# Optimization experiments

Hardware: AMD Instinct MI355X
Metric: run time of the kernel (lower is better)

The kernel has to match this reference:

```python
import jax, jax.numpy as jnp
import numpy as np

D = 128
N0, N1, N2 = 1048576, 131072, 8192   # node counts per sampled layer (src->tgt)
E0, E1 = 1048576, 131072             # edges per layer


def setup_inputs() -> dict:
    key = jax.random.key(0)
    ks = jax.random.split(key, 11)
    s = 1.0 / np.sqrt(D)  # torch Linear init scale
    u = lambda k: jax.random.uniform(k, (D, D), jnp.float32, -s, s)
    return {
        "x": jax.random.normal(ks[0], (N0, D), jnp.float32),
        "Wl0": u(ks[1]), "bl0": jnp.zeros((D,), jnp.float32), "Wr0": u(ks[2]),
        "Wl1": u(ks[3]), "bl1": jnp.zeros((D,), jnp.float32), "Wr1": u(ks[4]),
        "src0": jax.random.randint(ks[5], (E0,), 0, N0, jnp.int32),
        "dst0": jax.random.randint(ks[6], (E0,), 0, N1, jnp.int32),
        "src1": jax.random.randint(ks[7], (E1,), 0, N1, jnp.int32),
        "dst1": jax.random.randint(ks[8], (E1,), 0, N2, jnp.int32),
    }


def _sage_conv(x_src, x_tgt, src, dst, Wl, bl, Wr, n_tgt):
    # message: gather source features along edges; aggregate: mean per target
    msg = x_src[src]                                        # [E, D]
    agg = jax.ops.segment_sum(msg, dst, num_segments=n_tgt)  # [n_tgt, D]
    cnt = jax.ops.segment_sum(jnp.ones((src.shape[0], 1), x_src.dtype),
                              dst, num_segments=n_tgt)       # [n_tgt, 1]
    mean = agg / jnp.maximum(cnt, 1.0)                      # zero-degree -> 0
    return mean @ Wl + bl + x_tgt @ Wr


def reference(x, Wl0, bl0, Wr0, Wl1, bl1, Wr1, src0, dst0, src1, dst1):
    # layer 0: N0 sources -> N1 targets
    h = _sage_conv(x, x[:N1], src0, dst0, Wl0, bl0, Wr0, N1)
    h = jax.nn.relu(h)  # dropout p=0.0 is identity
    # layer 1: N1 sources -> N2 targets
    h = _sage_conv(h, h[:N2], src1, dst1, Wl1, bl1, Wr1, N2)
    return jax.nn.relu(h)
```

## Files before the change

kernel.cpp:

```cpp
#include <hip/hip_runtime.h>
#include <hip/hip_bf16.h>

#define D 128
#define N0_ 1048576
#define N1_ 131072
#define N2_ 8192
#define E0_ 1048576
#define E1_ 131072

typedef float f32x4 __attribute__((ext_vector_type(4)));
typedef short bf16x8 __attribute__((ext_vector_type(8)));
typedef unsigned short u16x4 __attribute__((ext_vector_type(4)));

__device__ __forceinline__ short f2bf(float f) {
    __hip_bfloat16 h = __float2bfloat16(f);
    return __builtin_bit_cast(short, h);
}
__device__ __forceinline__ float bf2f(short s) {
    return __bfloat162float(__builtin_bit_cast(__hip_bfloat16, s));
}

__global__ __launch_bounds__(256) void zero_kernel(int4* __restrict__ p, int n4) {
    int i = blockIdx.x * 256 + threadIdx.x;
    if (i < n4) p[i] = int4{0, 0, 0, 0};
}

__global__ __launch_bounds__(256) void hist_both(const int* __restrict__ dst0,
                                                 const int* __restrict__ dst1,
                                                 int* __restrict__ deg) {
    int g = blockIdx.x * 256 + threadIdx.x;
    if (g < E0_ / 4) {
        int4 d4 = ((const int4*)dst0)[g];
        atomicAdd(&deg[d4.x], 1);
        atomicAdd(&deg[d4.y], 1);
        atomicAdd(&deg[d4.z], 1);
        atomicAdd(&deg[d4.w], 1);
    } else {
        int4 d4 = ((const int4*)dst1)[g - E0_ / 4];
        atomicAdd(&deg[N1_ + d4.x], 1);
        atomicAdd(&deg[N1_ + d4.y], 1);
        atomicAdd(&deg[N1_ + d4.z], 1);
        atomicAdd(&deg[N1_ + d4.w], 1);
    }
}

__global__ __launch_bounds__(256) void scan1(const int* __restrict__ deg,
                                             int* __restrict__ offs,
                                             int* __restrict__ bsum, int n) {
    __shared__ int ws[4];
    int i = blockIdx.x * 256 + threadIdx.x;
    int lane = threadIdx.x & 63, wid = threadIdx.x >> 6;
    int v = (i < n) ? deg[i] : 0;
    int incl = v;
#pragma unroll
    for (int d = 1; d < 64; d <<= 1) {
        int u = __shfl_up(incl, d);
        if (lane >= d) incl += u;
    }
    if (lane == 63) ws[wid] = incl;
    __syncthreads();
    if (threadIdx.x == 0) {
        int a = 0;
        for (int w = 0; w < 4; ++w) { int t = ws[w]; ws[w] = a; a += t; }
        bsum[blockIdx.x] = a;
    }
    __syncthreads();
    if (i < n) offs[i] = incl - v + ws[wid];
}

__global__ __launch_bounds__(1024) void scan2(int* __restrict__ bsum, int nb) {
    __shared__ int ws[16];
    int i = threadIdx.x, lane = i & 63, wid = i >> 6;
    int v = (i < nb) ? bsum[i] : 0;
    int incl = v;
#pragma unroll
    for (int d = 1; d < 64; d <<= 1) {
        int u = __shfl_up(incl, d);
        if (lane >= d) incl += u;
    }
    if (lane == 63) ws[wid] = incl;
    __syncthreads();
    if (i == 0) {
        int a = 0;
        for (int w = 0; w < 16; ++w) { int t = ws[w]; ws[w] = a; a += t; }
    }
    __syncthreads();
    if (i < nb) bsum[i] = incl - v + ws[wid];
}

__global__ __launch_bounds__(256) void scan3(int* __restrict__ offs,
                                             const int* __restrict__ bsum, int n) {
    int i = blockIdx.x * 256 + threadIdx.x;
    if (i < n) offs[i] += bsum[blockIdx.x];
}

__global__ __launch_bounds__(256) void scatter_both(const int* __restrict__ src0,
                                                    const int* __restrict__ dst0,
                                                    const int* __restrict__ src1,
                                                    const int* __restrict__ dst1,
                                                    int* __restrict__ offs,
                                                    int* __restrict__ eidx0,
                                                    int* __restrict__ eidx1) {
    int g = blockIdx.x * 256 + threadIdx.x;
    if (g < E0_ / 4) {
        int4 s4 = ((const int4*)src0)[g];
        int4 d4 = ((const int4*)dst0)[g];
        int p;
        p = atomicAdd(&offs[d4.x], 1); eidx0[p] = s4.x;
        p = atomicAdd(&offs[d4.y], 1); eidx0[p] = s4.y;
        p = atomicAdd(&offs[d4.z], 1); eidx0[p] = s4.z;
        p = atomicAdd(&offs[d4.w], 1); eidx0[p] = s4.w;
    } else {
        int gq = g - E0_ / 4;
        int4 s4 = ((const int4*)src1)[gq];
        int4 d4 = ((const int4*)dst1)[gq];
        int p;
        p = atomicAdd(&offs[N1_ + d4.x], 1); eidx1[p - E0_] = s4.x;
        p = atomicAdd(&offs[N1_ + d4.y], 1); eidx1[p - E0_] = s4.y;
        p = atomicAdd(&offs[N1_ + d4.z], 1); eidx1[p - E0_] = s4.z;
        p = atomicAdd(&offs[N1_ + d4.w], 1); eidx1[p - E0_] = s4.w;
    }
}

template <bool SRCBF16>
__device__ __forceinline__ f32x4 row_load4(const void* xsrc_v, int s, int hl) {
    if (SRCBF16) {
        const short* xs = (const short*)xsrc_v;
        u16x4 v = ((const u16x4*)(xs + (size_t)s * D))[hl];
        f32x4 r;
        r[0] = bf2f((short)v[0]); r[1] = bf2f((short)v[1]);
        r[2] = bf2f((short)v[2]); r[3] = bf2f((short)v[3]);
        return r;
    } else {
        const float* xs = (const float*)xsrc_v;
        return ((const f32x4*)(xs + (size_t)s * D))[hl];
    }
}

template <bool SRCBF16>
__global__ __launch_bounds__(256) void aggregate(const void* __restrict__ xsrc_v,
                                                 const int* __restrict__ eidx,
                                                 const int* __restrict__ offs_end,
                                                 const int* __restrict__ deg,
                                                 int joint_base, int eidx_sub,
                                                 short* __restrict__ mean, int ntgt) {
    const int lane = threadIdx.x & 63;
    const int half = lane >> 5, hl = lane & 31;
    const int gw = (blockIdx.x * 256 + threadIdx.x) >> 6;
    const int nw = (gridDim.x * 256) >> 6;
    for (int t = gw; t < ntgt; t += nw) {
        const int tj = joint_base + t;
        const int dgr = deg[tj];
        const int start = offs_end[tj] - dgr - eidx_sub;
        f32x4 acc = {0.0f, 0.0f, 0.0f, 0.0f};
        for (int base = 0; base < dgr; base += 64) {
            const int nc = min(64, dgr - base);
            int sidx = (lane < nc) ? eidx[start + base + lane] : 0;
            int i = 0;
            for (; i + 8 <= nc; i += 8) {
                f32x4 v[4];
#pragma unroll
                for (int u = 0; u < 4; ++u) {
                    int s0 = __shfl(sidx, i + 2 * u);
                    int s1 = __shfl(sidx, i + 2 * u + 1);
                    v[u] = row_load4<SRCBF16>(xsrc_v, half ? s1 : s0, hl);
                }
#pragma unroll
                for (int u = 0; u < 4; ++u) acc += v[u];
            }
            for (; i + 2 <= nc; i += 2) {
                int s0 = __shfl(sidx, i);
                int s1 = __shfl(sidx, i + 1);
                acc += row_load4<SRCBF16>(xsrc_v, half ? s1 : s0, hl);
            }
            if (i < nc) {
                int s0 = __shfl(sidx, i);
                if (half == 0) acc += row_load4<SRCBF16>(xsrc_v, s0, hl);
            }
        }
#pragma unroll
        for (int c = 0; c < 4; ++c) acc[c] += __shfl_xor(acc[c], 32);
        const float r = (dgr > 0) ? 1.0f / (float)dgr : 0.0f;
        if (half == 0) {
            u16x4 o;
#pragma unroll
            for (int c = 0; c < 4; ++c) o[c] = (unsigned short)f2bf(acc[c] * r);
            ((u16x4*)(mean + (size_t)t * D))[hl] = o;
        }
    }
}

template <bool XBF16, bool OUTBF16>
__global__ __launch_bounds__(256) void sage_update(
    const short* __restrict__ mean, const void* __restrict__ xtgt_v,
    const float* __restrict__ Wl, const float* __restrict__ Wr,
    const float* __restrict__ bl, void* __restrict__ out_v, int ntiles) {
    __shared__ __align__(16) char wt[128 * 256 * 2];

    {
        int t = threadIdx.x;
        int j = t & 127;
        int half = t >> 7;
        const float* W = half ? Wr : Wl;
        for (int k = 0; k < 128; ++k) {
            float v = W[k * 128 + j];
            int kk = half * 128 + k;
            int byte = (j * 512 + kk * 2) ^ ((j & 7) << 4);
            *reinterpret_cast<short*>(wt + byte) = f2bf(v);
        }
    }
    __syncthreads();

    const int wave = threadIdx.x >> 6, lane = threadIdx.x & 63;
    const int rl = lane & 15;
    const int kq = lane >> 4;

    float blv[8];
#pragma unroll
    for (int nt = 0; nt < 8; ++nt) blv[nt] = bl[nt * 16 + rl];

    for (int tile = blockIdx.x; tile < ntiles; tile += gridDim.x) {
        const int grow = tile * 64 + wave * 16 + rl;
        f32x4 acc[8] = {};

#pragma unroll
        for (int ks = 0; ks < 8; ++ks) {
            const int k0 = ks * 32 + kq * 8;
            bf16x8 af;
            if (ks < 4) {
                af = *reinterpret_cast<const bf16x8*>(mean + (size_t)grow * D + k0);
            } else {
                const int kx = k0 - 128;
                if (XBF16) {
                    af = *reinterpret_cast<const bf16x8*>(
                        (const short*)xtgt_v + (size_t)grow * D + kx);
                } else {
                    const float4* p = reinterpret_cast<const float4*>(
                        (const float*)xtgt_v + (size_t)grow * D + kx);
                    float4 a = p[0], b = p[1];
                    af[0] = f2bf(a.x); af[1] = f2bf(a.y);
                    af[2] = f2bf(a.z); af[3] = f2bf(a.w);
                    af[4] = f2bf(b.x); af[5] = f2bf(b.y);
                    af[6] = f2bf(b.z); af[7] = f2bf(b.w);
                }
            }
#pragma unroll
            for (int nt = 0; nt < 8; ++nt) {
                const int j = nt * 16 + rl;
                const int byte = (j * 512 + k0 * 2) ^ ((j & 7) << 4);
                bf16x8 bfr = *reinterpret_cast<const bf16x8*>(wt + byte);
                acc[nt] =
                    __builtin_amdgcn_mfma_f32_16x16x32_bf16(af, bfr, acc[nt], 0, 0, 0);
            }
        }

        const int orow_base = tile * 64 + wave * 16 + kq * 4;
#pragma unroll
        for (int nt = 0; nt < 8; ++nt) {
            const int col = nt * 16 + rl;
#pragma unroll
            for (int r = 0; r < 4; ++r) {
                float v = acc[nt][r] + blv[nt];
                v = fmaxf(v, 0.0f);
                const size_t idx = (size_t)(orow_base + r) * D + col;
                if (OUTBF16)
                    ((short*)out_v)[idx] = f2bf(v);
                else
                    ((float*)out_v)[idx] = v;
            }
        }
    }
}

extern "C" void kernel_launch(void* const* d_in, const int* in_sizes, int n_in,
                              void* d_out, int out_size, void* d_ws, size_t ws_size,
                              hipStream_t stream) {
    const float* x   = (const float*)d_in[0];
    const float* Wl0 = (const float*)d_in[1];
    const float* bl0 = (const float*)d_in[2];
    const float* Wr0 = (const float*)d_in[3];
    const float* Wl1 = (const float*)d_in[4];
    const float* bl1 = (const float*)d_in[5];
    const float* Wr1 = (const float*)d_in[6];
    const int* src0  = (const int*)d_in[7];
    const int* dst0  = (const int*)d_in[8];
    const int* src1  = (const int*)d_in[9];
    const int* dst1  = (const int*)d_in[10];

    char* ws = (char*)d_ws;
    int*   deg   = (int*)(ws);
    int*   offs  = (int*)(ws + 557056);
    int*   bsum  = (int*)(ws + 1114112);
    int*   eidx0 = (int*)(ws + 1118208);
    int*   eidx1 = (int*)(ws + 5312512);
    short* mean0 = (short*)(ws + 5836800);
    short* mean1 = (short*)(ws + 39391232);
    short* h     = (short*)(ws + 41488384);

    const int NJ = N1_ + N2_;

    zero_kernel<<<136, 256, 0, stream>>>((int4*)deg, NJ / 4);
    hist_both<<<(E0_ + E1_) / 1024, 256, 0, stream>>>(dst0, dst1, deg);
    scan1<<<NJ / 256, 256, 0, stream>>>(deg, offs, bsum, NJ);
    scan2<<<1, 1024, 0, stream>>>(bsum, NJ / 256);
    scan3<<<NJ / 256, 256, 0, stream>>>(offs, bsum, NJ);
    scatter_both<<<(E0_ + E1_) / 1024, 256, 0, stream>>>(src0, dst0, src1, dst1,
                                                         offs, eidx0, eidx1);

    aggregate<false><<<4096, 256, 0, stream>>>(x, eidx0, offs, deg, 0, 0, mean0, N1_);
    sage_update<false, true><<<1024, 256, 0, stream>>>(
        mean0, x, Wl0, Wr0, bl0, h, N1_ / 64);

    aggregate<true><<<2048, 256, 0, stream>>>(h, eidx1, offs, deg, N1_, E0_, mean1, N2_);
    sage_update<true, false><<<128, 256, 0, stream>>>(
        mean1, h, Wl1, Wr1, bl1, d_out, N2_ / 64);
}
```

Baseline: 319.3 us.

## Pre-convert source features to bf16 fused with degree histogram

Adds a combined kernel in which most blocks convert the whole fp32 feature matrix to bf16 while the remaining blocks compute the in-degree histogram. The layer-0 aggregate and update kernels then read bf16 rows, halving the bytes of each random row gather. The cost is a full streaming read of the fp32 input plus a bf16 write of the same rows. Each source row is gathered only about once on average, so this conversion pass may cost more traffic than the gathers save. Summing bf16-rounded inputs also adds a small amount of precision loss.

```diff
diff --git a/kernel.cpp b/kernel.cpp
--- a/kernel.cpp
+++ b/kernel.cpp
@@ -8,6 +8,9 @@
 #define E0_ 1048576
 #define E1_ 131072
 
+#define CONVB 3584
+#define HISTB 512
+
 typedef float f32x4 __attribute__((ext_vector_type(4)));
 typedef short bf16x8 __attribute__((ext_vector_type(8)));
 typedef unsigned short u16x4 __attribute__((ext_vector_type(4)));
@@ -25,22 +28,39 @@
     if (i < n4) p[i] = int4{0, 0, 0, 0};
 }
 
-__global__ __launch_bounds__(256) void hist_both(const int* __restrict__ dst0,
-                                                 const int* __restrict__ dst1,
-                                                 int* __restrict__ deg) {
-    int g = blockIdx.x * 256 + threadIdx.x;
-    if (g < E0_ / 4) {
-        int4 d4 = ((const int4*)dst0)[g];
-        atomicAdd(&deg[d4.x], 1);
-        atomicAdd(&deg[d4.y], 1);
-        atomicAdd(&deg[d4.z], 1);
-        atomicAdd(&deg[d4.w], 1);
+__global__ __launch_bounds__(256) void conv_hist(
+    const f32x4* __restrict__ x4, u16x4* __restrict__ xbf4,
+    const int* __restrict__ dst0, const int* __restrict__ dst1,
+    int* __restrict__ deg) {
+    if (blockIdx.x < CONVB) {
+        const int n4 = N0_ * D / 4;
+        for (int i = blockIdx.x * 256 + threadIdx.x; i < n4; i += CONVB * 256) {
+            f32x4 v = x4[i];
+            u16x4 o;
+            o[0] = (unsigned short)f2bf(v[0]);
+            o[1] = (unsigned short)f2bf(v[1]);
+            o[2] = (unsigned short)f2bf(v[2]);
+            o[3] = (unsigned short)f2bf(v[3]);
+            xbf4[i] = o;
+        }
     } else {
-        int4 d4 = ((const int4*)dst1)[g - E0_ / 4];
-        atomicAdd(&deg[N1_ + d4.x], 1);
-        atomicAdd(&deg[N1_ + d4.y], 1);
-        atomicAdd(&deg[N1_ + d4.z], 1);
-        atomicAdd(&deg[N1_ + d4.w], 1);
+        const int nq0 = E0_ / 4, nq = (E0_ + E1_) / 4;
+        for (int g = (blockIdx.x - CONVB) * 256 + threadIdx.x; g < nq;
+             g += HISTB * 256) {
+            if (g < nq0) {
+                int4 d4 = ((const int4*)dst0)[g];
+                atomicAdd(&deg[d4.x], 1);
+                atomicAdd(&deg[d4.y], 1);
+                atomicAdd(&deg[d4.z], 1);
+                atomicAdd(&deg[d4.w], 1);
+            } else {
+                int4 d4 = ((const int4*)dst1)[g - nq0];
+                atomicAdd(&deg[N1_ + d4.x], 1);
+                atomicAdd(&deg[N1_ + d4.y], 1);
+                atomicAdd(&deg[N1_ + d4.z], 1);
+                atomicAdd(&deg[N1_ + d4.w], 1);
+            }
+        }
     }
 }
 
@@ -122,23 +142,15 @@
     }
 }
 
-template <bool SRCBF16>
-__device__ __forceinline__ f32x4 row_load4(const void* xsrc_v, int s, int hl) {
-    if (SRCBF16) {
-        const short* xs = (const short*)xsrc_v;
-        u16x4 v = ((const u16x4*)(xs + (size_t)s * D))[hl];
-        f32x4 r;
-        r[0] = bf2f((short)v[0]); r[1] = bf2f((short)v[1]);
-        r[2] = bf2f((short)v[2]); r[3] = bf2f((short)v[3]);
-        return r;
-    } else {
-        const float* xs = (const float*)xsrc_v;
-        return ((const f32x4*)(xs + (size_t)s * D))[hl];
-    }
-}
-
-template <bool SRCBF16>
-__global__ __launch_bounds__(256) void aggregate(const void* __restrict__ xsrc_v,
+__device__ __forceinline__ f32x4 row_load4(const short* xs, int s, int hl) {
+    u16x4 v = ((const u16x4*)(xs + (size_t)s * D))[hl];
+    f32x4 r;
+    r[0] = bf2f((short)v[0]); r[1] = bf2f((short)v[1]);
+    r[2] = bf2f((short)v[2]); r[3] = bf2f((short)v[3]);
+    return r;
+}
+
+__global__ __launch_bounds__(256) void aggregate(const short* __restrict__ xsrc,
                                                  const int* __restrict__ eidx,
                                                  const int* __restrict__ offs_end,
                                                  const int* __restrict__ deg,
@@ -163,7 +175,7 @@
                 for (int u = 0; u < 4; ++u) {
                     int s0 = __shfl(sidx, i + 2 * u);
                     int s1 = __shfl(sidx, i + 2 * u + 1);
-                    v[u] = row_load4<SRCBF16>(xsrc_v, half ? s1 : s0, hl);
+                    v[u] = row_load4(xsrc, half ? s1 : s0, hl);
                 }
 #pragma unroll
                 for (int u = 0; u < 4; ++u) acc += v[u];
@@ -171,11 +183,11 @@
             for (; i + 2 <= nc; i += 2) {
                 int s0 = __shfl(sidx, i);
                 int s1 = __shfl(sidx, i + 1);
-                acc += row_load4<SRCBF16>(xsrc_v, half ? s1 : s0, hl);
+                acc += row_load4(xsrc, half ? s1 : s0, hl);
             }
             if (i < nc) {
                 int s0 = __shfl(sidx, i);
-                if (half == 0) acc += row_load4<SRCBF16>(xsrc_v, s0, hl);
+                if (half == 0) acc += row_load4(xsrc, s0, hl);
             }
         }
 #pragma unroll
@@ -190,9 +202,9 @@
     }
 }
 
-template <bool XBF16, bool OUTBF16>
+template <bool OUTBF16>
 __global__ __launch_bounds__(256) void sage_update(
-    const short* __restrict__ mean, const void* __restrict__ xtgt_v,
+    const short* __restrict__ mean, const short* __restrict__ xtgt,
     const float* __restrict__ Wl, const float* __restrict__ Wr,
     const float* __restrict__ bl, void* __restrict__ out_v, int ntiles) {
     __shared__ __align__(16) char wt[128 * 256 * 2];
@@ -230,19 +242,7 @@
             if (ks < 4) {
                 af = *reinterpret_cast<const bf16x8*>(mean + (size_t)grow * D + k0);
             } else {
-                const int kx = k0 - 128;
-                if (XBF16) {
-                    af = *reinterpret_cast<const bf16x8*>(
-                        (const short*)xtgt_v + (size_t)grow * D + kx);
-                } else {
-                    const float4* p = reinterpret_cast<const float4*>(
-                        (const float*)xtgt_v + (size_t)grow * D + kx);
-                    float4 a = p[0], b = p[1];
-                    af[0] = f2bf(a.x); af[1] = f2bf(a.y);
-                    af[2] = f2bf(a.z); af[3] = f2bf(a.w);
-                    af[4] = f2bf(b.x); af[5] = f2bf(b.y);
-                    af[6] = f2bf(b.z); af[7] = f2bf(b.w);
-                }
+                af = *reinterpret_cast<const bf16x8*>(xtgt + (size_t)grow * D + k0 - 128);
             }
 #pragma unroll
             for (int nt = 0; nt < 8; ++nt) {
@@ -296,22 +296,24 @@
     short* mean0 = (short*)(ws + 5836800);
     short* mean1 = (short*)(ws + 39391232);
     short* h     = (short*)(ws + 41488384);
+    short* xbf   = (short*)(ws + 75042816);
 
     const int NJ = N1_ + N2_;
 
     zero_kernel<<<136, 256, 0, stream>>>((int4*)deg, NJ / 4);
-    hist_both<<<(E0_ + E1_) / 1024, 256, 0, stream>>>(dst0, dst1, deg);
+    conv_hist<<<CONVB + HISTB, 256, 0, stream>>>(
+        (const f32x4*)x, (u16x4*)xbf, dst0, dst1, deg);
     scan1<<<NJ / 256, 256, 0, stream>>>(deg, offs, bsum, NJ);
     scan2<<<1, 1024, 0, stream>>>(bsum, NJ / 256);
     scan3<<<NJ / 256, 256, 0, stream>>>(offs, bsum, NJ);
     scatter_both<<<(E0_ + E1_) / 1024, 256, 0, stream>>>(src0, dst0, src1, dst1,
                                                          offs, eidx0, eidx1);
 
-    aggregate<false><<<4096, 256, 0, stream>>>(x, eidx0, offs, deg, 0, 0, mean0, N1_);
-    sage_update<false, true><<<1024, 256, 0, stream>>>(
-        mean0, x, Wl0, Wr0, bl0, h, N1_ / 64);
-
-    aggregate<true><<<2048, 256, 0, stream>>>(h, eidx1, offs, deg, N1_, E0_, mean1, N2_);
-    sage_update<true, false><<<128, 256, 0, stream>>>(
+    aggregate<<<4096, 256, 0, stream>>>(xbf, eidx0, offs, deg, 0, 0, mean0, N1_);
+    sage_update<true><<<1024, 256, 0, stream>>>(
+        mean0, xbf, Wl0, Wr0, bl0, h, N1_ / 64);
+
+    aggregate<<<2048, 256, 0, stream>>>(h, eidx1, offs, deg, N1_, E0_, mean1, N2_);
+    sage_update<false><<<128, 256, 0, stream>>>(
         mean1, h, Wl1, Wr1, bl1, d_out, N2_ / 64);
 }
```

After: 407.9 us. +27.8%, slower.

## Fold scan fixup into consumers and aggregate one target per half-wave

Applied to the files above, without the earlier changes.

The third scan pass is removed: the block prefix from bsum is now added where offsets are read, in scatter and aggregate. The zero kernel becomes a hipMemsetAsync. Aggregation now gives each 32-lane half-wave its own target with 8 row loads in flight, which drops the cross-half shuffle reduction and the idle half on odd degrees. The second aggregate grid is halved. This saves two launches and improves load parallelism, at the cost of an extra bsum lookup per edge in scatter.

```diff
diff --git a/kernel.cpp b/kernel.cpp
--- a/kernel.cpp
+++ b/kernel.cpp
@@ -18,11 +18,6 @@
 }
 __device__ __forceinline__ float bf2f(short s) {
     return __bfloat162float(__builtin_bit_cast(__hip_bfloat16, s));
-}
-
-__global__ __launch_bounds__(256) void zero_kernel(int4* __restrict__ p, int n4) {
-    int i = blockIdx.x * 256 + threadIdx.x;
-    if (i < n4) p[i] = int4{0, 0, 0, 0};
 }
 
 __global__ __launch_bounds__(256) void hist_both(const int* __restrict__ dst0,
@@ -88,17 +83,12 @@
     if (i < nb) bsum[i] = incl - v + ws[wid];
 }
 
-__global__ __launch_bounds__(256) void scan3(int* __restrict__ offs,
-                                             const int* __restrict__ bsum, int n) {
-    int i = blockIdx.x * 256 + threadIdx.x;
-    if (i < n) offs[i] += bsum[blockIdx.x];
-}
-
 __global__ __launch_bounds__(256) void scatter_both(const int* __restrict__ src0,
                                                     const int* __restrict__ dst0,
                                                     const int* __restrict__ src1,
                                                     const int* __restrict__ dst1,
                                                     int* __restrict__ offs,
+                                                    const int* __restrict__ bsum,
                                                     int* __restrict__ eidx0,
                                                     int* __restrict__ eidx1) {
     int g = blockIdx.x * 256 + threadIdx.x;
@@ -106,19 +96,19 @@
         int4 s4 = ((const int4*)src0)[g];
         int4 d4 = ((const int4*)dst0)[g];
         int p;
-        p = atomicAdd(&offs[d4.x], 1); eidx0[p] = s4.x;
-        p = atomicAdd(&offs[d4.y], 1); eidx0[p] = s4.y;
-        p = atomicAdd(&offs[d4.z], 1); eidx0[p] = s4.z;
-        p = atomicAdd(&offs[d4.w], 1); eidx0[p] = s4.w;
+        p = atomicAdd(&offs[d4.x], 1) + bsum[d4.x >> 8]; eidx0[p] = s4.x;
+        p = atomicAdd(&offs[d4.y], 1) + bsum[d4.y >> 8]; eidx0[p] = s4.y;
+        p = atomicAdd(&offs[d4.z], 1) + bsum[d4.z >> 8]; eidx0[p] = s4.z;
+        p = atomicAdd(&offs[d4.w], 1) + bsum[d4.w >> 8]; eidx0[p] = s4.w;
     } else {
         int gq = g - E0_ / 4;
         int4 s4 = ((const int4*)src1)[gq];
         int4 d4 = ((const int4*)dst1)[gq];
-        int p;
-        p = atomicAdd(&offs[N1_ + d4.x], 1); eidx1[p - E0_] = s4.x;
-        p = atomicAdd(&offs[N1_ + d4.y], 1); eidx1[p - E0_] = s4.y;
-        p = atomicAdd(&offs[N1_ + d4.z], 1); eidx1[p - E0_] = s4.z;
-        p = atomicAdd(&offs[N1_ + d4.w], 1); eidx1[p - E0_] = s4.w;
+        int j, p;
+        j = N1_ + d4.x; p = atomicAdd(&offs[j], 1) + bsum[j >> 8]; eidx1[p - E0_] = s4.x;
+        j = N1_ + d4.y; p = atomicAdd(&offs[j], 1) + bsum[j >> 8]; eidx1[p - E0_] = s4.y;
+        j = N1_ + d4.z; p = atomicAdd(&offs[j], 1) + bsum[j >> 8]; eidx1[p - E0_] = s4.z;
+        j = N1_ + d4.w; p = atomicAdd(&offs[j], 1) + bsum[j >> 8]; eidx1[p - E0_] = s4.w;
     }
 }
 
@@ -140,53 +130,53 @@
 template <bool SRCBF16>
 __global__ __launch_bounds__(256) void aggregate(const void* __restrict__ xsrc_v,
                                                  const int* __restrict__ eidx,
-                                                 const int* __restrict__ offs_end,
+                                                 const int* __restrict__ offs,
                                                  const int* __restrict__ deg,
+                                                 const int* __restrict__ bsum,
                                                  int joint_base, int eidx_sub,
                                                  short* __restrict__ mean, int ntgt) {
     const int lane = threadIdx.x & 63;
-    const int half = lane >> 5, hl = lane & 31;
-    const int gw = (blockIdx.x * 256 + threadIdx.x) >> 6;
-    const int nw = (gridDim.x * 256) >> 6;
-    for (int t = gw; t < ntgt; t += nw) {
+    const int hl = lane & 31;
+    const int hsel = lane & 32;
+    const int ghw = (blockIdx.x * 256 + threadIdx.x) >> 5;
+    const int nhw = (gridDim.x * 256) >> 5;
+    for (int t = ghw; t < ntgt; t += nhw) {
         const int tj = joint_base + t;
         const int dgr = deg[tj];
-        const int start = offs_end[tj] - dgr - eidx_sub;
+        const int start = offs[tj] - dgr + bsum[tj >> 8] - eidx_sub;
         f32x4 acc = {0.0f, 0.0f, 0.0f, 0.0f};
-        for (int base = 0; base < dgr; base += 64) {
-            const int nc = min(64, dgr - base);
-            int sidx = (lane < nc) ? eidx[start + base + lane] : 0;
+        for (int base = 0; base < dgr; base += 32) {
+            const int nc = min(32, dgr - base);
+            int sidx = (hl < nc) ? eidx[start + base + hl] : 0;
             int i = 0;
             for (; i + 8 <= nc; i += 8) {
-                f32x4 v[4];
-#pragma unroll
-                for (int u = 0; u < 4; ++u) {
-                    int s0 = __shfl(sidx, i + 2 * u);
-                    int s1 = __shfl(sidx, i + 2 * u + 1);
-                    v[u] = row_load4<SRCBF16>(xsrc_v, half ? s1 : s0, hl);
+                f32x4 v[8];
+#pragma unroll
+                for (int u = 0; u < 8; ++u) {
+                    int s = __shfl(sidx, hsel + i + u);
+                    v[u] = row_load4<SRCBF16>(xsrc_v, s, hl);
                 }
 #pragma unroll
-                for (int u = 0; u < 4; ++u) acc += v[u];
+                for (int u = 0; u < 8; ++u) acc += v[u];
             }
             for (; i + 2 <= nc; i += 2) {
-                int s0 = __shfl(sidx, i);
-                int s1 = __shfl(sidx, i + 1);
-                acc += row_load4<SRCBF16>(xsrc_v, half ? s1 : s0, hl);
+                int s0 = __shfl(sidx, hsel + i);
+                int s1 = __shfl(sidx, hsel + i + 1);
+                f32x4 v0 = row_load4<SRCBF16>(xsrc_v, s0, hl);
+                f32x4 v1 = row_load4<SRCBF16>(xsrc_v, s1, hl);
+                acc += v0;
+                acc += v1;
             }
             if (i < nc) {
-                int s0 = __shfl(sidx, i);
-                if (half == 0) acc += row_load4<SRCBF16>(xsrc_v, s0, hl);
+                int s0 = __shfl(sidx, hsel + i);
+                acc += row_load4<SRCBF16>(xsrc_v, s0, hl);
             }
         }
-#pragma unroll
-        for (int c = 0; c < 4; ++c) acc[c] += __shfl_xor(acc[c], 32);
         const float r = (dgr > 0) ? 1.0f / (float)dgr : 0.0f;
-        if (half == 0) {
-            u16x4 o;
-#pragma unroll
-            for (int c = 0; c < 4; ++c) o[c] = (unsigned short)f2bf(acc[c] * r);
-            ((u16x4*)(mean + (size_t)t * D))[hl] = o;
-        }
+        u16x4 o;
+#pragma unroll
+        for (int c = 0; c < 4; ++c) o[c] = (unsigned short)f2bf(acc[c] * r);
+        ((u16x4*)(mean + (size_t)t * D))[hl] = o;
     }
 }
 
@@ -299,19 +289,20 @@
 
     const int NJ = N1_ + N2_;
 
-    zero_kernel<<<136, 256, 0, stream>>>((int4*)deg, NJ / 4);
+    hipMemsetAsync(deg, 0, 557056, stream);
     hist_both<<<(E0_ + E1_) / 1024, 256, 0, stream>>>(dst0, dst1, deg);
     scan1<<<NJ / 256, 256, 0, stream>>>(deg, offs, bsum, NJ);
     scan2<<<1, 1024, 0, stream>>>(bsum, NJ / 256);
-    scan3<<<NJ / 256, 256, 0, stream>>>(offs, bsum, NJ);
     scatter_both<<<(E0_ + E1_) / 1024, 256, 0, stream>>>(src0, dst0, src1, dst1,
-                                                         offs, eidx0, eidx1);
-
-    aggregate<false><<<4096, 256, 0, stream>>>(x, eidx0, offs, deg, 0, 0, mean0, N1_);
+                                                         offs, bsum, eidx0, eidx1);
+
+    aggregate<false><<<4096, 256, 0, stream>>>(x, eidx0, offs, deg, bsum, 0, 0,
+                                               mean0, N1_);
     sage_update<false, true><<<1024, 256, 0, stream>>>(
         mean0, x, Wl0, Wr0, bl0, h, N1_ / 64);
 
-    aggregate<true><<<2048, 256, 0, stream>>>(h, eidx1, offs, deg, N1_, E0_, mean1, N2_);
+    aggregate<true><<<1024, 256, 0, stream>>>(h, eidx1, offs, deg, bsum, N1_, E0_,
+                                              mean1, N2_);
     sage_update<true, false><<<128, 256, 0, stream>>>(
         mean1, h, Wl1, Wr1, bl1, d_out, N2_ / 64);
 }
```

After: 318.2 us. About the same (-0.3%).
